# Kernel tuning notes

Hardware: AMD Instinct MI355X
Metric: run time of the kernel (lower is better)

## Reference

```python
import jax, jax.numpy as jnp
import numpy as np

N = 50000        # nodes
E = 800000       # edges
IN_DIM, HID, OUT = 512, 256, 128
EPS = 1e-5       # PyG LayerNorm eps (added to std)


def setup_inputs() -> dict:
    key = jax.random.key(0)
    ks = jax.random.split(key, 24)
    def lin(k, i, o, scale=0.05):
        kw, kb = jax.random.split(k)
        return (jax.random.normal(kw, (i, o), jnp.float32) * scale,
                jax.random.normal(kb, (o,), jnp.float32) * scale)
    x = jax.random.normal(ks[0], (N, IN_DIM), jnp.float32)
    edge_index = jax.random.randint(ks[1], (2, E), 0, N, jnp.int64)
    Wq1, bq1 = lin(ks[2], IN_DIM, HID)
    Wk1, bk1 = lin(ks[3], IN_DIM, HID)
    Wv1, bv1 = lin(ks[4], IN_DIM, HID)
    Ws1, bs1 = lin(ks[5], IN_DIM, HID)
    g1 = jnp.ones((HID,), jnp.float32)
    be1 = jnp.zeros((HID,), jnp.float32)
    Wq2, bq2 = lin(ks[6], HID, OUT)
    Wk2, bk2 = lin(ks[7], HID, OUT)
    Wv2, bv2 = lin(ks[8], HID, OUT)
    Ws2, bs2 = lin(ks[9], HID, OUT)
    g2 = jnp.ones((OUT,), jnp.float32)
    be2 = jnp.zeros((OUT,), jnp.float32)
    return dict(x=x, Wq1=Wq1, bq1=bq1, Wk1=Wk1, bk1=bk1, Wv1=Wv1, bv1=bv1,
                Ws1=Ws1, bs1=bs1, g1=g1, be1=be1,
                Wq2=Wq2, bq2=bq2, Wk2=Wk2, bk2=bk2, Wv2=Wv2, bv2=bv2,
                Ws2=Ws2, bs2=bs2, g2=g2, be2=be2, edge_index=edge_index)


def transformer_conv(x, edge_index, Wq, bq, Wk, bk, Wv, bv, Ws, bs):
    # PyG TransformerConv, heads=1, concat=True, root_weight=True
    src, dst = edge_index[0], edge_index[1]
    n = x.shape[0]
    d = Wq.shape[1]
    q = x @ Wq + bq                               # [N, d]
    k = x @ Wk + bk
    v = x @ Wv + bv
    score = (q[dst] * k[src]).sum(-1) / jnp.sqrt(jnp.asarray(d, x.dtype))  # [E]
    m = jax.ops.segment_max(score, dst, num_segments=n)     # per-target max
    e = jnp.exp(score - m[dst])
    denom = jax.ops.segment_sum(e, dst, num_segments=n)
    alpha = e / denom[dst]                         # scatter-softmax over in-edges
    agg = jax.ops.segment_sum(alpha[:, None] * v[src], dst, num_segments=n)
    return agg + (x @ Ws + bs)                     # root/skip connection


def graph_layer_norm(h, w, b):
    # PyG LayerNorm mode='graph', no batch: normalize over ALL entries
    h = h - h.mean()
    return h / (h.std() + EPS) * w + b


def reference(x, Wq1, bq1, Wk1, bk1, Wv1, bv1, Ws1, bs1, g1, be1,
              Wq2, bq2, Wk2, bk2, Wv2, bv2, Ws2, bs2, g2, be2, edge_index):
    a1 = graph_layer_norm(
        transformer_conv(x, edge_index, Wq1, bq1, Wk1, bk1, Wv1, bv1, Ws1, bs1),
        g1, be1)
    h1 = jax.nn.elu(a1)  # ELU(alpha=1.0)
    h2 = graph_layer_norm(
        transformer_conv(h1, edge_index, Wq2, bq2, Wk2, bk2, Wv2, bv2, Ws2, bs2),
        g2, be2)
    return h2
```

## Files before the change

### kernel.cpp

```cpp
#include <hip/hip_runtime.h>
#include <stdint.h>
#include <math.h>

#define IN_DIM 512
#define HID    256
#define OUTD   128
#define LN_EPS 1e-5f

typedef unsigned short u16;
typedef unsigned int   u32;
typedef short short8 __attribute__((ext_vector_type(8)));
typedef float f32x4  __attribute__((ext_vector_type(4)));

__device__ __forceinline__ float bf2f(u32 h) {
  union { u32 u; float f; } c; c.u = h << 16; return c.f;
}
__device__ __forceinline__ u16 f2bf(float f) {
  union { float f; u32 u; } c; c.f = f;
  u32 u = c.u;
  return (u16)((u + 0x7FFFu + ((u >> 16) & 1u)) >> 16);
}

__device__ __forceinline__ void gload_lds16(const void* g, void* l) {
  __builtin_amdgcn_global_load_lds((const __attribute__((address_space(1))) void*)g,
                                   (__attribute__((address_space(3))) void*)l, 16, 0, 0);
}

__global__ void k_prep(const float* __restrict__ x, u16* __restrict__ x_bf, int n4,
                       const float* __restrict__ bq1, const float* __restrict__ bk1,
                       const float* __restrict__ bv1, const float* __restrict__ bs1,
                       const float* __restrict__ bq2, const float* __restrict__ bk2,
                       const float* __restrict__ bv2, const float* __restrict__ bs2,
                       float* __restrict__ bc1, float* __restrict__ bc2) {
  int id = blockIdx.x * blockDim.x + threadIdx.x;
  if (id < n4) {
    const float4 v = ((const float4*)x)[id];
    ushort4 o;
    o.x = f2bf(v.x); o.y = f2bf(v.y); o.z = f2bf(v.z); o.w = f2bf(v.w);
    ((ushort4*)x_bf)[id] = o;
    return;
  }
  id -= n4;
  if (id < 4 * HID) {
    const float* s = (id < HID) ? bq1 : (id < 2 * HID) ? bk1 : (id < 3 * HID) ? bv1 : bs1;
    bc1[id] = s[id & (HID - 1)];
    return;
  }
  id -= 4 * HID;
  if (id < 4 * OUTD) {
    const float* s = (id < OUTD) ? bq2 : (id < 2 * OUTD) ? bk2 : (id < 3 * OUTD) ? bv2 : bs2;
    bc2[id] = s[id & (OUTD - 1)];
  }
}

__global__ void k_transpose4(const float* __restrict__ s0, const float* __restrict__ s1,
                             const float* __restrict__ s2, const float* __restrict__ s3,
                             u16* __restrict__ out, int K, int Nw) {
  __shared__ u16 t[32][33];
  const float* src = (blockIdx.z == 0) ? s0 : (blockIdx.z == 1) ? s1
                     : (blockIdx.z == 2) ? s2 : s3;
  u16* dst = out + (size_t)blockIdx.z * K * Nw;
  int k0 = blockIdx.x * 32, n0 = blockIdx.y * 32;
  int tx = threadIdx.x, ty = threadIdx.y;
#pragma unroll
  for (int i = 0; i < 32; i += 8)
    t[ty + i][tx] = f2bf(src[(size_t)(k0 + ty + i) * Nw + n0 + tx]);
  __syncthreads();
#pragma unroll
  for (int i = 0; i < 32; i += 8)
    dst[(size_t)(n0 + ty + i) * K + k0 + tx] = t[tx][ty + i];
}

__global__ void k_hist(const int* __restrict__ dst, int* __restrict__ deg, int E) {
  int e = blockIdx.x * blockDim.x + threadIdx.x;
  if (e < E) atomicAdd(&deg[dst[e]], 1);
}

__global__ void k_block_sum(const int* __restrict__ deg, int* __restrict__ bsum, int n) {
  __shared__ int sm[256];
  int i = blockIdx.x * 256 + threadIdx.x;
  sm[threadIdx.x] = (i < n) ? deg[i] : 0;
  __syncthreads();
  for (int off = 128; off > 0; off >>= 1) {
    if (threadIdx.x < off) sm[threadIdx.x] += sm[threadIdx.x + off];
    __syncthreads();
  }
  if (threadIdx.x == 0) bsum[blockIdx.x] = sm[0];
}

__global__ void k_scan_bsum(const int* __restrict__ bsum, int* __restrict__ boff, int nb) {
  __shared__ int sm[256];
  int t = threadIdx.x;
  int v = (t < nb) ? bsum[t] : 0;
  sm[t] = v;
  __syncthreads();
  for (int off = 1; off < 256; off <<= 1) {
    int tmp = (t >= off) ? sm[t - off] : 0;
    __syncthreads();
    sm[t] += tmp;
    __syncthreads();
  }
  if (t < nb) boff[t] = sm[t] - v;
}

__global__ void k_scan_final(const int* __restrict__ deg, const int* __restrict__ boff,
                             int* __restrict__ offsets, int* __restrict__ cur,
                             int n, int total) {
  __shared__ int sm[256];
  int t = threadIdx.x;
  int i = blockIdx.x * 256 + t;
  int v = (i < n) ? deg[i] : 0;
  sm[t] = v;
  __syncthreads();
  for (int off = 1; off < 256; off <<= 1) {
    int tmp = (t >= off) ? sm[t - off] : 0;
    __syncthreads();
    sm[t] += tmp;
    __syncthreads();
  }
  if (i < n) {
    int o = boff[blockIdx.x] + sm[t] - v;
    offsets[i] = o;
    cur[i] = o;
  }
  if (i == 0) offsets[n] = total;
}

__global__ void k_scatter(const int* __restrict__ src, const int* __restrict__ dst,
                          int* __restrict__ cursor, int* __restrict__ ssrc, int E) {
  int e = blockIdx.x * blockDim.x + threadIdx.x;
  if (e >= E) return;
  int d = dst[e];
  int pos = atomicAdd(&cursor[d], 1);
  ssrc[pos] = src[e];
}

__global__ __launch_bounds__(256) void k_gemm_bf16_nt(
    const u16* __restrict__ A, const u16* __restrict__ Bt, const float* __restrict__ bias,
    u16* __restrict__ C, int M, int K, int Nt) {
  __shared__ __align__(16) u16 As[128 * 32];
  __shared__ __align__(16) u16 Bs[128 * 32];
  const int tid = threadIdx.x;
  const int bm0 = blockIdx.x * 128;
  const int bn0 = blockIdx.y * 128;
  const int wave = tid >> 6, lane = tid & 63;
  const int q = lane >> 4, r16 = lane & 15;
  const int wm = (wave >> 1) * 64, wn = (wave & 1) * 64;

  f32x4 acc[4][4];
#pragma unroll
  for (int i = 0; i < 4; i++)
#pragma unroll
    for (int j = 0; j < 4; j++) acc[i][j] = (f32x4){0.f, 0.f, 0.f, 0.f};

  const int r0 = tid >> 2;
  const int c0 = (tid & 3) * 8;

  for (int kt = 0; kt < K; kt += 32) {
#pragma unroll
    for (int h = 0; h < 2; ++h) {
      int row = r0 + h * 64;
      gload_lds16(A + (size_t)(bm0 + row) * K + kt + c0, &As[row * 32 + c0]);
      gload_lds16(Bt + (size_t)(bn0 + row) * K + kt + c0, &Bs[row * 32 + c0]);
    }
    __syncthreads();
    short8 af[4], bfr[4];
#pragma unroll
    for (int i = 0; i < 4; i++) af[i] = *(const short8*)(&As[(wm + i * 16 + r16) * 32 + q * 8]);
#pragma unroll
    for (int j = 0; j < 4; j++) bfr[j] = *(const short8*)(&Bs[(wn + j * 16 + r16) * 32 + q * 8]);
#pragma unroll
    for (int i = 0; i < 4; i++)
#pragma unroll
      for (int j = 0; j < 4; j++)
        acc[i][j] = __builtin_amdgcn_mfma_f32_16x16x32_bf16(af[i], bfr[j], acc[i][j], 0, 0, 0);
    __syncthreads();
  }

#pragma unroll
  for (int i = 0; i < 4; i++) {
#pragma unroll
    for (int r = 0; r < 4; r++) {
      int grow = bm0 + wm + i * 16 + q * 4 + r;
      if (grow >= M) continue;
      size_t rbase = (size_t)grow * Nt;
#pragma unroll
      for (int j = 0; j < 4; j++) {
        int gcol = bn0 + wn + j * 16 + r16;
        float v = acc[i][j][r] + bias[gcol];
        C[rbase + gcol] = f2bf(v);
      }
    }
  }
}

template <int VPL>
__device__ __forceinline__ void load_bf(const u16* __restrict__ p, int lane, float* f) {
  if constexpr (VPL == 4) {
    uint2 r = *(const uint2*)(p + lane * 4);
    f[0] = bf2f(r.x & 0xffffu); f[1] = bf2f(r.x >> 16);
    f[2] = bf2f(r.y & 0xffffu); f[3] = bf2f(r.y >> 16);
  } else {
    u32 r = *(const u32*)(p + lane * 2);
    f[0] = bf2f(r & 0xffffu); f[1] = bf2f(r >> 16);
  }
}

template <int H, bool OUT_BF16>
__global__ __launch_bounds__(256) void k_conv(
    const u16* __restrict__ qkvs, const int* __restrict__ offsets,
    const int* __restrict__ ssrc, u16* __restrict__ out_bf,
    float* __restrict__ out_f, int n, float scale) {
  constexpr int VPL = H / 64;
  int gw = (blockIdx.x * blockDim.x + threadIdx.x) >> 6;
  int lane = threadIdx.x & 63;
  if (gw >= n) return;
  const u16* base = qkvs + (size_t)gw * (4 * H);
  float qf[VPL];
  load_bf<VPL>(base, lane, qf);
  int beg = offsets[gw], end = offsets[gw + 1];
  float m = -INFINITY, l = 0.f;
  float agg[VPL];
#pragma unroll
  for (int w = 0; w < VPL; w++) agg[w] = 0.f;

  int i = beg;
  for (; i + 4 <= end; i += 4) {
    int s0 = ssrc[i], s1 = ssrc[i + 1], s2 = ssrc[i + 2], s3 = ssrc[i + 3];
    const u16* k0p = qkvs + (size_t)s0 * (4 * H) + H;
    const u16* k1p = qkvs + (size_t)s1 * (4 * H) + H;
    const u16* k2p = qkvs + (size_t)s2 * (4 * H) + H;
    const u16* k3p = qkvs + (size_t)s3 * (4 * H) + H;
    float k0[VPL], k1[VPL], k2[VPL], k3[VPL];
    float v0[VPL], v1[VPL], v2[VPL], v3[VPL];
    load_bf<VPL>(k0p, lane, k0);
    load_bf<VPL>(k1p, lane, k1);
    load_bf<VPL>(k2p, lane, k2);
    load_bf<VPL>(k3p, lane, k3);
    load_bf<VPL>(k0p + H, lane, v0);
    load_bf<VPL>(k1p + H, lane, v1);
    load_bf<VPL>(k2p + H, lane, v2);
    load_bf<VPL>(k3p + H, lane, v3);
    float d0 = 0.f, d1 = 0.f, d2 = 0.f, d3 = 0.f;
#pragma unroll
    for (int w = 0; w < VPL; w++) {
      d0 += qf[w] * k0[w]; d1 += qf[w] * k1[w];
      d2 += qf[w] * k2[w]; d3 += qf[w] * k3[w];
    }
#pragma unroll
    for (int off = 32; off > 0; off >>= 1) {
      d0 += __shfl_xor(d0, off, 64);
      d1 += __shfl_xor(d1, off, 64);
      d2 += __shfl_xor(d2, off, 64);
      d3 += __shfl_xor(d3, off, 64);
    }
    d0 *= scale; d1 *= scale; d2 *= scale; d3 *= scale;
    float cm = fmaxf(fmaxf(d0, d1), fmaxf(d2, d3));
    float nm = fmaxf(m, cm);
    float sc = __expf(m - nm);
    float p0 = __expf(d0 - nm), p1 = __expf(d1 - nm);
    float p2 = __expf(d2 - nm), p3 = __expf(d3 - nm);
    m = nm;
    l = l * sc + (p0 + p1) + (p2 + p3);
#pragma unroll
    for (int w = 0; w < VPL; w++)
      agg[w] = agg[w] * sc + p0 * v0[w] + p1 * v1[w] + p2 * v2[w] + p3 * v3[w];
  }
  for (; i < end; ++i) {
    int s = ssrc[i];
    const u16* kb = qkvs + (size_t)s * (4 * H) + H;
    float kf[VPL], vf[VPL];
    load_bf<VPL>(kb, lane, kf);
    load_bf<VPL>(kb + H, lane, vf);
    float d = 0.f;
#pragma unroll
    for (int w = 0; w < VPL; w++) d += qf[w] * kf[w];
#pragma unroll
    for (int off = 32; off > 0; off >>= 1) d += __shfl_xor(d, off, 64);
    float score = d * scale;
    float nm = fmaxf(m, score);
    float sc = __expf(m - nm);
    float p = __expf(score - nm);
    m = nm;
    l = l * sc + p;
#pragma unroll
    for (int w = 0; w < VPL; w++) agg[w] = agg[w] * sc + p * vf[w];
  }

  float sf[VPL];
  load_bf<VPL>(base + 3 * H, lane, sf);
  float inv = (end > beg) ? 1.f / l : 0.f;
#pragma unroll
  for (int w = 0; w < VPL; w++) {
    float r = agg[w] * inv + sf[w];
    if (OUT_BF16) out_bf[(size_t)gw * H + lane * VPL + w] = f2bf(r);
    else out_f[(size_t)gw * H + lane * VPL + w] = r;
  }
}

__global__ void k_stats_bf16(const u16* __restrict__ a, int n8, double* __restrict__ st) {
  float s = 0.f, s2 = 0.f;
  for (int i = blockIdx.x * blockDim.x + threadIdx.x; i < n8; i += gridDim.x * blockDim.x) {
    uint4 v = ((const uint4*)a)[i];
    const u32 va[4] = {v.x, v.y, v.z, v.w};
#pragma unroll
    for (int w = 0; w < 4; w++) {
      float x0 = bf2f(va[w] & 0xffffu), x1 = bf2f(va[w] >> 16);
      s += x0 + x1; s2 += x0 * x0 + x1 * x1;
    }
  }
  __shared__ float sm[256], sm2[256];
  sm[threadIdx.x] = s; sm2[threadIdx.x] = s2;
  __syncthreads();
  for (int off = 128; off > 0; off >>= 1) {
    if (threadIdx.x < off) { sm[threadIdx.x] += sm[threadIdx.x + off]; sm2[threadIdx.x] += sm2[threadIdx.x + off]; }
    __syncthreads();
  }
  if (threadIdx.x == 0) { atomicAdd(&st[0], (double)sm[0]); atomicAdd(&st[1], (double)sm2[0]); }
}

__global__ void k_stats_f32(const float* __restrict__ a, int n4, double* __restrict__ st) {
  float s = 0.f, s2 = 0.f;
  for (int i = blockIdx.x * blockDim.x + threadIdx.x; i < n4; i += gridDim.x * blockDim.x) {
    float4 v = ((const float4*)a)[i];
    s += v.x + v.y + v.z + v.w;
    s2 += v.x * v.x + v.y * v.y + v.z * v.z + v.w * v.w;
  }
  __shared__ float sm[256], sm2[256];
  sm[threadIdx.x] = s; sm2[threadIdx.x] = s2;
  __syncthreads();
  for (int off = 128; off > 0; off >>= 1) {
    if (threadIdx.x < off) { sm[threadIdx.x] += sm[threadIdx.x + off]; sm2[threadIdx.x] += sm2[threadIdx.x + off]; }
    __syncthreads();
  }
  if (threadIdx.x == 0) { atomicAdd(&st[0], (double)sm[0]); atomicAdd(&st[1], (double)sm2[0]); }
}

__global__ void k_finstats(const double* __restrict__ st, float* __restrict__ fs, double cnt) {
  double mu = st[0] / cnt;
  double var = st[1] / cnt - mu * mu;
  if (var < 0.0) var = 0.0;
  fs[0] = (float)mu;
  fs[1] = (float)(1.0 / (sqrt(var) + (double)LN_EPS));
}

__global__ void k_norm_elu_bf16(const u16* __restrict__ a, const float* __restrict__ g,
                                const float* __restrict__ b, const float* __restrict__ fs,
                                u16* __restrict__ out, int n8, int Hmask) {
  int id = blockIdx.x * blockDim.x + threadIdx.x;
  if (id >= n8) return;
  int i8 = id * 8;
  int cb = i8 & Hmask;
  uint4 v = *(const uint4*)(a + i8);
  const u32 va[4] = {v.x, v.y, v.z, v.w};
  float mu = fs[0], inv = fs[1];
  uint4 o;
  u32* op = (u32*)&o;
#pragma unroll
  for (int w = 0; w < 4; w++) {
    float y0 = (bf2f(va[w] & 0xffffu) - mu) * inv * g[cb + 2 * w] + b[cb + 2 * w];
    float y1 = (bf2f(va[w] >> 16) - mu) * inv * g[cb + 2 * w + 1] + b[cb + 2 * w + 1];
    y0 = (y0 > 0.f) ? y0 : (__expf(y0) - 1.f);
    y1 = (y1 > 0.f) ? y1 : (__expf(y1) - 1.f);
    op[w] = (u32)f2bf(y0) | ((u32)f2bf(y1) << 16);
  }
  *(uint4*)(out + i8) = o;
}

__global__ void k_norm_f32(float* __restrict__ a, const float* __restrict__ g,
                           const float* __restrict__ b, const float* __restrict__ fs,
                           int n4, int Hmask) {
  int id = blockIdx.x * blockDim.x + threadIdx.x;
  if (id >= n4) return;
  int i4 = id * 4;
  int cb = i4 & Hmask;
  float4 v = *(const float4*)(a + i4);
  float mu = fs[0], inv = fs[1];
  float4 o;
  o.x = (v.x - mu) * inv * g[cb] + b[cb];
  o.y = (v.y - mu) * inv * g[cb + 1] + b[cb + 1];
  o.z = (v.z - mu) * inv * g[cb + 2] + b[cb + 2];
  o.w = (v.w - mu) * inv * g[cb + 3] + b[cb + 3];
  *(float4*)(a + i4) = o;
}

extern "C" void kernel_launch(void* const* d_in, const int* in_sizes, int n_in,
                              void* d_out, int out_size, void* d_ws, size_t ws_size,
                              hipStream_t stream) {
  const float* x   = (const float*)d_in[0];
  const float* Wq1 = (const float*)d_in[1];  const float* bq1 = (const float*)d_in[2];
  const float* Wk1 = (const float*)d_in[3];  const float* bk1 = (const float*)d_in[4];
  const float* Wv1 = (const float*)d_in[5];  const float* bv1 = (const float*)d_in[6];
  const float* Ws1 = (const float*)d_in[7];  const float* bs1 = (const float*)d_in[8];
  const float* g1  = (const float*)d_in[9];  const float* be1 = (const float*)d_in[10];
  const float* Wq2 = (const float*)d_in[11]; const float* bq2 = (const float*)d_in[12];
  const float* Wk2 = (const float*)d_in[13]; const float* bk2 = (const float*)d_in[14];
  const float* Wv2 = (const float*)d_in[15]; const float* bv2 = (const float*)d_in[16];
  const float* Ws2 = (const float*)d_in[17]; const float* bs2 = (const float*)d_in[18];
  const float* g2  = (const float*)d_in[19]; const float* be2 = (const float*)d_in[20];
  const int*   ei  = (const int*)d_in[21];

  const int N = in_sizes[0] / IN_DIM;
  const int E = in_sizes[21] / 2;
  const int* esrc = ei;
  const int* edst = ei + E;

  char* w = (char*)d_ws;
  auto carve = [&](size_t bytes) { char* p = w; w += (bytes + 255) & ~(size_t)255; return p; };
  int* deg   = (int*)carve((size_t)(N + 1) * 4);
  double* st = (double*)carve(64);
  u16* x_bf  = (u16*)carve((size_t)N * IN_DIM * 2);
  u16* Wt1   = (u16*)carve((size_t)4 * HID * IN_DIM * 2);
  u16* Wt2   = (u16*)carve((size_t)4 * OUTD * HID * 2);
  float* bc1 = (float*)carve(4 * HID * 4);
  float* bc2 = (float*)carve(4 * OUTD * 4);
  u16* qkvs1 = (u16*)carve((size_t)N * 4 * HID * 2);
  u16* a1    = (u16*)carve((size_t)N * HID * 2);
  int* offs  = (int*)carve((size_t)(N + 1) * 4);
  int* cur   = (int*)carve((size_t)(N + 1) * 4);
  int* ssrc  = (int*)carve((size_t)E * 4);
  int* bsum  = (int*)carve(1024);
  int* boff  = (int*)carve(1024);
  float* fs  = (float*)carve(64);
  u16* h1    = x_bf;
  u16* qkvs2 = qkvs1;

  hipMemsetAsync(deg, 0, (size_t)((char*)st - (char*)deg) + 64, stream);

  int n4 = N * IN_DIM / 4;
  int prep_total = n4 + 4 * HID + 4 * OUTD;
  k_prep<<<(prep_total + 255) / 256, 256, 0, stream>>>(
      x, x_bf, n4, bq1, bk1, bv1, bs1, bq2, bk2, bv2, bs2, bc1, bc2);
  dim3 tb(32, 8);
  dim3 tg1(IN_DIM / 32, HID / 32, 4);
  k_transpose4<<<tg1, tb, 0, stream>>>(Wq1, Wk1, Wv1, Ws1, Wt1, IN_DIM, HID);
  dim3 tg2(HID / 32, OUTD / 32, 4);
  k_transpose4<<<tg2, tb, 0, stream>>>(Wq2, Wk2, Wv2, Ws2, Wt2, HID, OUTD);

  int nb = (N + 255) / 256;
  k_hist<<<(E + 255) / 256, 256, 0, stream>>>(edst, deg, E);
  k_block_sum<<<nb, 256, 0, stream>>>(deg, bsum, N);
  k_scan_bsum<<<1, 256, 0, stream>>>(bsum, boff, nb);
  k_scan_final<<<nb, 256, 0, stream>>>(deg, boff, offs, cur, N, E);
  k_scatter<<<(E + 255) / 256, 256, 0, stream>>>(esrc, edst, cur, ssrc, E);

  dim3 gg1((N + 127) / 128, (4 * HID) / 128);
  k_gemm_bf16_nt<<<gg1, 256, 0, stream>>>(x_bf, Wt1, bc1, qkvs1, N, IN_DIM, 4 * HID);
  k_conv<HID, true><<<(N + 3) / 4, 256, 0, stream>>>(qkvs1, offs, ssrc, a1, nullptr, N,
                                                     1.0f / sqrtf((float)HID));
  k_stats_bf16<<<2048, 256, 0, stream>>>(a1, N * HID / 8, st);
  k_finstats<<<1, 1, 0, stream>>>(st, fs, (double)N * HID);
  k_norm_elu_bf16<<<(N * HID / 8 + 255) / 256, 256, 0, stream>>>(a1, g1, be1, fs, h1,
                                                                 N * HID / 8, HID - 1);

  dim3 gg2((N + 127) / 128, (4 * OUTD) / 128);
  k_gemm_bf16_nt<<<gg2, 256, 0, stream>>>(h1, Wt2, bc2, qkvs2, N, HID, 4 * OUTD);
  k_conv<OUTD, false><<<(N + 3) / 4, 256, 0, stream>>>(qkvs2, offs, ssrc, nullptr, (float*)d_out,
                                                       N, 1.0f / sqrtf((float)OUTD));
  k_stats_f32<<<2048, 256, 0, stream>>>((const float*)d_out, N * OUTD / 4, st + 2);
  k_finstats<<<1, 1, 0, stream>>>(st + 2, fs + 2, (double)N * OUTD);
  k_norm_f32<<<(N * OUTD / 4 + 255) / 256, 256, 0, stream>>>((float*)d_out, g2, be2, fs + 2,
                                                             N * OUTD / 4, OUTD - 1);
}
```

Before: 734.1 us.

## Fuse prep kernels, single-block scan, merge scatter into GEMM, fold stats into conv

Merges the x conversion, degree histogram, bias copy and both weight transposes into one multi-role launch. Replaces the three-kernel prefix scan with a single 1024-thread block scan. Appends the CSR scatter blocks to the first GEMM grid and remaps GEMM tiles with an XCD-aware swizzle. Computes the LayerNorm sum and sum of squares inside the conv kernel from its register results, and has the norm kernels derive mean and std from the raw sums, which removes the separate stats and finstats kernels. The cost is a serial single-block scan and extra per-block double atomics in conv. There is also an ordering risk: the scatter writes ssrc while sharing a launch with the GEMM, which is safe only because the GEMM does not read ssrc.

```diff
diff --git a/kernel.cpp b/kernel.cpp
--- a/kernel.cpp
+++ b/kernel.cpp
@@ -26,123 +26,136 @@
                                    (__attribute__((address_space(3))) void*)l, 16, 0, 0);
 }
 
-__global__ void k_prep(const float* __restrict__ x, u16* __restrict__ x_bf, int n4,
-                       const float* __restrict__ bq1, const float* __restrict__ bk1,
-                       const float* __restrict__ bv1, const float* __restrict__ bs1,
-                       const float* __restrict__ bq2, const float* __restrict__ bk2,
-                       const float* __restrict__ bv2, const float* __restrict__ bs2,
-                       float* __restrict__ bc1, float* __restrict__ bc2) {
-  int id = blockIdx.x * blockDim.x + threadIdx.x;
-  if (id < n4) {
-    const float4 v = ((const float4*)x)[id];
-    ushort4 o;
-    o.x = f2bf(v.x); o.y = f2bf(v.y); o.z = f2bf(v.z); o.w = f2bf(v.w);
-    ((ushort4*)x_bf)[id] = o;
+__global__ __launch_bounds__(256) void k_prep(
+    const float* __restrict__ x, u16* __restrict__ x_bf, int n4,
+    const int* __restrict__ edst, int* __restrict__ deg, int E,
+    const float* __restrict__ bq1, const float* __restrict__ bk1,
+    const float* __restrict__ bv1, const float* __restrict__ bs1,
+    const float* __restrict__ bq2, const float* __restrict__ bk2,
+    const float* __restrict__ bv2, const float* __restrict__ bs2,
+    float* __restrict__ bc1, float* __restrict__ bc2,
+    const float* __restrict__ Wq1, const float* __restrict__ Wk1,
+    const float* __restrict__ Wv1, const float* __restrict__ Ws1,
+    const float* __restrict__ Wq2, const float* __restrict__ Wk2,
+    const float* __restrict__ Wv2, const float* __restrict__ Ws2,
+    u16* __restrict__ Wt1, u16* __restrict__ Wt2,
+    int b_cvt, int b_hist) {
+  __shared__ u16 t[32][33];
+  int blk = blockIdx.x;
+  int tid = threadIdx.x;
+  if (blk < b_cvt) {
+    int id = blk * 256 + tid;
+    if (id < n4) {
+      const float4 v = ((const float4*)x)[id];
+      ushort4 o;
+      o.x = f2bf(v.x); o.y = f2bf(v.y); o.z = f2bf(v.z); o.w = f2bf(v.w);
+      ((ushort4*)x_bf)[id] = o;
+    }
     return;
   }
-  id -= n4;
-  if (id < 4 * HID) {
-    const float* s = (id < HID) ? bq1 : (id < 2 * HID) ? bk1 : (id < 3 * HID) ? bv1 : bs1;
-    bc1[id] = s[id & (HID - 1)];
+  blk -= b_cvt;
+  if (blk < b_hist) {
+    int e = blk * 256 + tid;
+    if (e < E) atomicAdd(&deg[edst[e]], 1);
     return;
   }
-  id -= 4 * HID;
-  if (id < 4 * OUTD) {
-    const float* s = (id < OUTD) ? bq2 : (id < 2 * OUTD) ? bk2 : (id < 3 * OUTD) ? bv2 : bs2;
-    bc2[id] = s[id & (OUTD - 1)];
-  }
-}
-
-__global__ void k_transpose4(const float* __restrict__ s0, const float* __restrict__ s1,
-                             const float* __restrict__ s2, const float* __restrict__ s3,
-                             u16* __restrict__ out, int K, int Nw) {
-  __shared__ u16 t[32][33];
-  const float* src = (blockIdx.z == 0) ? s0 : (blockIdx.z == 1) ? s1
-                     : (blockIdx.z == 2) ? s2 : s3;
-  u16* dst = out + (size_t)blockIdx.z * K * Nw;
-  int k0 = blockIdx.x * 32, n0 = blockIdx.y * 32;
-  int tx = threadIdx.x, ty = threadIdx.y;
-#pragma unroll
-  for (int i = 0; i < 32; i += 8)
-    t[ty + i][tx] = f2bf(src[(size_t)(k0 + ty + i) * Nw + n0 + tx]);
+  blk -= b_hist;
+  if (blk < 6) {
+    int id = blk * 256 + tid;
+    if (id < 4 * HID) {
+      const float* s = (id < HID) ? bq1 : (id < 2 * HID) ? bk1 : (id < 3 * HID) ? bv1 : bs1;
+      bc1[id] = s[id & (HID - 1)];
+    } else if (id < 4 * HID + 4 * OUTD) {
+      int j = id - 4 * HID;
+      const float* s = (j < OUTD) ? bq2 : (j < 2 * OUTD) ? bk2 : (j < 3 * OUTD) ? bv2 : bs2;
+      bc2[j] = s[j & (OUTD - 1)];
+    }
+    return;
+  }
+  blk -= 6;
+  int tx = tid & 31, ty = tid >> 5;
+  if (blk < 512) {
+    int mat = blk >> 7, r = blk & 127;
+    int k0 = (r >> 3) * 32, n0 = (r & 7) * 32;
+    const float* src = (mat == 0) ? Wq1 : (mat == 1) ? Wk1 : (mat == 2) ? Wv1 : Ws1;
+    u16* dst = Wt1 + (size_t)mat * IN_DIM * HID;
+#pragma unroll
+    for (int i = 0; i < 32; i += 8)
+      t[ty + i][tx] = f2bf(src[(size_t)(k0 + ty + i) * HID + n0 + tx]);
+    __syncthreads();
+#pragma unroll
+    for (int i = 0; i < 32; i += 8)
+      dst[(size_t)(n0 + ty + i) * IN_DIM + k0 + tx] = t[tx][ty + i];
+    return;
+  }
+  blk -= 512;
+  {
+    int mat = blk >> 5, r = blk & 31;
+    int k0 = (r >> 2) * 32, n0 = (r & 3) * 32;
+    const float* src = (mat == 0) ? Wq2 : (mat == 1) ? Wk2 : (mat == 2) ? Wv2 : Ws2;
+    u16* dst = Wt2 + (size_t)mat * HID * OUTD;
+#pragma unroll
+    for (int i = 0; i < 32; i += 8)
+      t[ty + i][tx] = f2bf(src[(size_t)(k0 + ty + i) * OUTD + n0 + tx]);
+    __syncthreads();
+#pragma unroll
+    for (int i = 0; i < 32; i += 8)
+      dst[(size_t)(n0 + ty + i) * HID + k0 + tx] = t[tx][ty + i];
+  }
+}
+
+__global__ __launch_bounds__(1024) void k_scan(const int* __restrict__ deg,
+                                               int* __restrict__ offsets,
+                                               int* __restrict__ cur, int n, int total) {
+  __shared__ int sm[1024];
+  int t = threadIdx.x;
+  int chunk = (n + 1023) / 1024;
+  int base = t * chunk;
+  int s = 0;
+  for (int i = base; i < base + chunk && i < n; ++i) s += deg[i];
+  sm[t] = s;
   __syncthreads();
-#pragma unroll
-  for (int i = 0; i < 32; i += 8)
-    dst[(size_t)(n0 + ty + i) * K + k0 + tx] = t[tx][ty + i];
-}
-
-__global__ void k_hist(const int* __restrict__ dst, int* __restrict__ deg, int E) {
-  int e = blockIdx.x * blockDim.x + threadIdx.x;
-  if (e < E) atomicAdd(&deg[dst[e]], 1);
-}
-
-__global__ void k_block_sum(const int* __restrict__ deg, int* __restrict__ bsum, int n) {
-  __shared__ int sm[256];
-  int i = blockIdx.x * 256 + threadIdx.x;
-  sm[threadIdx.x] = (i < n) ? deg[i] : 0;
-  __syncthreads();
-  for (int off = 128; off > 0; off >>= 1) {
-    if (threadIdx.x < off) sm[threadIdx.x] += sm[threadIdx.x + off];
-    __syncthreads();
-  }
-  if (threadIdx.x == 0) bsum[blockIdx.x] = sm[0];
-}
-
-__global__ void k_scan_bsum(const int* __restrict__ bsum, int* __restrict__ boff, int nb) {
-  __shared__ int sm[256];
-  int t = threadIdx.x;
-  int v = (t < nb) ? bsum[t] : 0;
-  sm[t] = v;
-  __syncthreads();
-  for (int off = 1; off < 256; off <<= 1) {
-    int tmp = (t >= off) ? sm[t - off] : 0;
-    __syncthreads();
-    sm[t] += tmp;
-    __syncthreads();
-  }
-  if (t < nb) boff[t] = sm[t] - v;
-}
-
-__global__ void k_scan_final(const int* __restrict__ deg, const int* __restrict__ boff,
-                             int* __restrict__ offsets, int* __restrict__ cur,
-                             int n, int total) {
-  __shared__ int sm[256];
-  int t = threadIdx.x;
-  int i = blockIdx.x * 256 + t;
-  int v = (i < n) ? deg[i] : 0;
-  sm[t] = v;
-  __syncthreads();
-  for (int off = 1; off < 256; off <<= 1) {
-    int tmp = (t >= off) ? sm[t - off] : 0;
-    __syncthreads();
-    sm[t] += tmp;
-    __syncthreads();
-  }
-  if (i < n) {
-    int o = boff[blockIdx.x] + sm[t] - v;
-    offsets[i] = o;
-    cur[i] = o;
-  }
-  if (i == 0) offsets[n] = total;
-}
-
-__global__ void k_scatter(const int* __restrict__ src, const int* __restrict__ dst,
-                          int* __restrict__ cursor, int* __restrict__ ssrc, int E) {
-  int e = blockIdx.x * blockDim.x + threadIdx.x;
-  if (e >= E) return;
-  int d = dst[e];
-  int pos = atomicAdd(&cursor[d], 1);
-  ssrc[pos] = src[e];
-}
-
-__global__ __launch_bounds__(256) void k_gemm_bf16_nt(
+  for (int off = 1; off < 1024; off <<= 1) {
+    int v = (t >= off) ? sm[t - off] : 0;
+    __syncthreads();
+    sm[t] += v;
+    __syncthreads();
+  }
+  int run = sm[t] - s;
+  for (int i = base; i < base + chunk && i < n; ++i) {
+    offsets[i] = run;
+    cur[i] = run;
+    run += deg[i];
+  }
+  if (t == 0) offsets[n] = total;
+}
+
+__global__ __launch_bounds__(256) void k_gemm_sc(
     const u16* __restrict__ A, const u16* __restrict__ Bt, const float* __restrict__ bias,
-    u16* __restrict__ C, int M, int K, int Nt) {
+    u16* __restrict__ C, int M, int K, int Nt, int nbn, int gemm_blocks,
+    const int* __restrict__ esrc, const int* __restrict__ edst,
+    int* __restrict__ cur, int* __restrict__ ssrc, int E) {
+  if ((int)blockIdx.x >= gemm_blocks) {
+    int e = (blockIdx.x - gemm_blocks) * 256 + threadIdx.x;
+    if (e < E) {
+      int d = edst[e];
+      int pos = atomicAdd(&cur[d], 1);
+      ssrc[pos] = esrc[e];
+    }
+    return;
+  }
+  int bid = blockIdx.x;
+  int xcd = bid & 7;
+  int nm = bid >> 3;
+  int n = nm % nbn;
+  int m = (nm / nbn) * 8 + xcd;
+  if (m * 128 >= M) return;
+
   __shared__ __align__(16) u16 As[128 * 32];
   __shared__ __align__(16) u16 Bs[128 * 32];
   const int tid = threadIdx.x;
-  const int bm0 = blockIdx.x * 128;
-  const int bn0 = blockIdx.y * 128;
+  const int bm0 = m * 128;
+  const int bn0 = n * 128;
   const int wave = tid >> 6, lane = tid & 63;
   const int q = lane >> 4, r16 = lane & 15;
   const int wm = (wave >> 1) * 64, wn = (wave & 1) * 64;
@@ -210,150 +223,134 @@
 __global__ __launch_bounds__(256) void k_conv(
     const u16* __restrict__ qkvs, const int* __restrict__ offsets,
     const int* __restrict__ ssrc, u16* __restrict__ out_bf,
-    float* __restrict__ out_f, int n, float scale) {
+    float* __restrict__ out_f, int n, float scale, double* __restrict__ st) {
   constexpr int VPL = H / 64;
   int gw = (blockIdx.x * blockDim.x + threadIdx.x) >> 6;
+  int wave = threadIdx.x >> 6;
   int lane = threadIdx.x & 63;
-  if (gw >= n) return;
-  const u16* base = qkvs + (size_t)gw * (4 * H);
-  float qf[VPL];
-  load_bf<VPL>(base, lane, qf);
-  int beg = offsets[gw], end = offsets[gw + 1];
-  float m = -INFINITY, l = 0.f;
-  float agg[VPL];
-#pragma unroll
-  for (int w = 0; w < VPL; w++) agg[w] = 0.f;
-
-  int i = beg;
-  for (; i + 4 <= end; i += 4) {
-    int s0 = ssrc[i], s1 = ssrc[i + 1], s2 = ssrc[i + 2], s3 = ssrc[i + 3];
-    const u16* k0p = qkvs + (size_t)s0 * (4 * H) + H;
-    const u16* k1p = qkvs + (size_t)s1 * (4 * H) + H;
-    const u16* k2p = qkvs + (size_t)s2 * (4 * H) + H;
-    const u16* k3p = qkvs + (size_t)s3 * (4 * H) + H;
-    float k0[VPL], k1[VPL], k2[VPL], k3[VPL];
-    float v0[VPL], v1[VPL], v2[VPL], v3[VPL];
-    load_bf<VPL>(k0p, lane, k0);
-    load_bf<VPL>(k1p, lane, k1);
-    load_bf<VPL>(k2p, lane, k2);
-    load_bf<VPL>(k3p, lane, k3);
-    load_bf<VPL>(k0p + H, lane, v0);
-    load_bf<VPL>(k1p + H, lane, v1);
-    load_bf<VPL>(k2p + H, lane, v2);
-    load_bf<VPL>(k3p + H, lane, v3);
-    float d0 = 0.f, d1 = 0.f, d2 = 0.f, d3 = 0.f;
-#pragma unroll
-    for (int w = 0; w < VPL; w++) {
-      d0 += qf[w] * k0[w]; d1 += qf[w] * k1[w];
-      d2 += qf[w] * k2[w]; d3 += qf[w] * k3[w];
-    }
-#pragma unroll
-    for (int off = 32; off > 0; off >>= 1) {
-      d0 += __shfl_xor(d0, off, 64);
-      d1 += __shfl_xor(d1, off, 64);
-      d2 += __shfl_xor(d2, off, 64);
-      d3 += __shfl_xor(d3, off, 64);
-    }
-    d0 *= scale; d1 *= scale; d2 *= scale; d3 *= scale;
-    float cm = fmaxf(fmaxf(d0, d1), fmaxf(d2, d3));
-    float nm = fmaxf(m, cm);
-    float sc = __expf(m - nm);
-    float p0 = __expf(d0 - nm), p1 = __expf(d1 - nm);
-    float p2 = __expf(d2 - nm), p3 = __expf(d3 - nm);
-    m = nm;
-    l = l * sc + (p0 + p1) + (p2 + p3);
-#pragma unroll
-    for (int w = 0; w < VPL; w++)
-      agg[w] = agg[w] * sc + p0 * v0[w] + p1 * v1[w] + p2 * v2[w] + p3 * v3[w];
-  }
-  for (; i < end; ++i) {
-    int s = ssrc[i];
-    const u16* kb = qkvs + (size_t)s * (4 * H) + H;
-    float kf[VPL], vf[VPL];
-    load_bf<VPL>(kb, lane, kf);
-    load_bf<VPL>(kb + H, lane, vf);
-    float d = 0.f;
-#pragma unroll
-    for (int w = 0; w < VPL; w++) d += qf[w] * kf[w];
-#pragma unroll
-    for (int off = 32; off > 0; off >>= 1) d += __shfl_xor(d, off, 64);
-    float score = d * scale;
-    float nm = fmaxf(m, score);
-    float sc = __expf(m - nm);
-    float p = __expf(score - nm);
-    m = nm;
-    l = l * sc + p;
-#pragma unroll
-    for (int w = 0; w < VPL; w++) agg[w] = agg[w] * sc + p * vf[w];
-  }
-
-  float sf[VPL];
-  load_bf<VPL>(base + 3 * H, lane, sf);
-  float inv = (end > beg) ? 1.f / l : 0.f;
-#pragma unroll
-  for (int w = 0; w < VPL; w++) {
-    float r = agg[w] * inv + sf[w];
-    if (OUT_BF16) out_bf[(size_t)gw * H + lane * VPL + w] = f2bf(r);
-    else out_f[(size_t)gw * H + lane * VPL + w] = r;
-  }
-}
-
-__global__ void k_stats_bf16(const u16* __restrict__ a, int n8, double* __restrict__ st) {
+  bool live = gw < n;
+  float r[VPL];
+#pragma unroll
+  for (int w = 0; w < VPL; w++) r[w] = 0.f;
+
+  if (live) {
+    const u16* base = qkvs + (size_t)gw * (4 * H);
+    float qf[VPL];
+    load_bf<VPL>(base, lane, qf);
+    int beg = offsets[gw], end = offsets[gw + 1];
+    float m = -INFINITY, l = 0.f;
+    float agg[VPL];
+#pragma unroll
+    for (int w = 0; w < VPL; w++) agg[w] = 0.f;
+
+    int i = beg;
+    for (; i + 4 <= end; i += 4) {
+      int s0 = ssrc[i], s1 = ssrc[i + 1], s2 = ssrc[i + 2], s3 = ssrc[i + 3];
+      const u16* k0p = qkvs + (size_t)s0 * (4 * H) + H;
+      const u16* k1p = qkvs + (size_t)s1 * (4 * H) + H;
+      const u16* k2p = qkvs + (size_t)s2 * (4 * H) + H;
+      const u16* k3p = qkvs + (size_t)s3 * (4 * H) + H;
+      float k0[VPL], k1[VPL], k2[VPL], k3[VPL];
+      float v0[VPL], v1[VPL], v2[VPL], v3[VPL];
+      load_bf<VPL>(k0p, lane, k0);
+      load_bf<VPL>(k1p, lane, k1);
+      load_bf<VPL>(k2p, lane, k2);
+      load_bf<VPL>(k3p, lane, k3);
+      load_bf<VPL>(k0p + H, lane, v0);
+      load_bf<VPL>(k1p + H, lane, v1);
+      load_bf<VPL>(k2p + H, lane, v2);
+      load_bf<VPL>(k3p + H, lane, v3);
+      float d0 = 0.f, d1 = 0.f, d2 = 0.f, d3 = 0.f;
+#pragma unroll
+      for (int w = 0; w < VPL; w++) {
+        d0 += qf[w] * k0[w]; d1 += qf[w] * k1[w];
+        d2 += qf[w] * k2[w]; d3 += qf[w] * k3[w];
+      }
+#pragma unroll
+      for (int off = 32; off > 0; off >>= 1) {
+        d0 += __shfl_xor(d0, off, 64);
+        d1 += __shfl_xor(d1, off, 64);
+        d2 += __shfl_xor(d2, off, 64);
+        d3 += __shfl_xor(d3, off, 64);
+      }
+      d0 *= scale; d1 *= scale; d2 *= scale; d3 *= scale;
+      float cm = fmaxf(fmaxf(d0, d1), fmaxf(d2, d3));
+      float nm = fmaxf(m, cm);
+      float sc = __expf(m - nm);
+      float p0 = __expf(d0 - nm), p1 = __expf(d1 - nm);
+      float p2 = __expf(d2 - nm), p3 = __expf(d3 - nm);
+      m = nm;
+      l = l * sc + (p0 + p1) + (p2 + p3);
+#pragma unroll
+      for (int w = 0; w < VPL; w++)
+        agg[w] = agg[w] * sc + p0 * v0[w] + p1 * v1[w] + p2 * v2[w] + p3 * v3[w];
+    }
+    for (; i < end; ++i) {
+      int s = ssrc[i];
+      const u16* kb = qkvs + (size_t)s * (4 * H) + H;
+      float kf[VPL], vf[VPL];
+      load_bf<VPL>(kb, lane, kf);
+      load_bf<VPL>(kb + H, lane, vf);
+      float d = 0.f;
+#pragma unroll
+      for (int w = 0; w < VPL; w++) d += qf[w] * kf[w];
+#pragma unroll
+      for (int off = 32; off > 0; off >>= 1) d += __shfl_xor(d, off, 64);
+      float score = d * scale;
+      float nm = fmaxf(m, score);
+      float sc = __expf(m - nm);
+      float p = __expf(score - nm);
+      m = nm;
+      l = l * sc + p;
+#pragma unroll
+      for (int w = 0; w < VPL; w++) agg[w] = agg[w] * sc + p * vf[w];
+    }
+
+    float sf[VPL];
+    load_bf<VPL>(base + 3 * H, lane, sf);
+    float inv = (end > beg) ? 1.f / l : 0.f;
+#pragma unroll
+    for (int w = 0; w < VPL; w++) r[w] = agg[w] * inv + sf[w];
+    if (OUT_BF16) {
+#pragma unroll
+      for (int w = 0; w < VPL; w++) out_bf[(size_t)gw * H + lane * VPL + w] = f2bf(r[w]);
+    } else {
+#pragma unroll
+      for (int w = 0; w < VPL; w++) out_f[(size_t)gw * H + lane * VPL + w] = r[w];
+    }
+  }
+
   float s = 0.f, s2 = 0.f;
-  for (int i = blockIdx.x * blockDim.x + threadIdx.x; i < n8; i += gridDim.x * blockDim.x) {
-    uint4 v = ((const uint4*)a)[i];
-    const u32 va[4] = {v.x, v.y, v.z, v.w};
-#pragma unroll
-    for (int w = 0; w < 4; w++) {
-      float x0 = bf2f(va[w] & 0xffffu), x1 = bf2f(va[w] >> 16);
-      s += x0 + x1; s2 += x0 * x0 + x1 * x1;
-    }
-  }
-  __shared__ float sm[256], sm2[256];
-  sm[threadIdx.x] = s; sm2[threadIdx.x] = s2;
+#pragma unroll
+  for (int w = 0; w < VPL; w++) { s += r[w]; s2 += r[w] * r[w]; }
+#pragma unroll
+  for (int off = 32; off > 0; off >>= 1) {
+    s += __shfl_xor(s, off, 64);
+    s2 += __shfl_xor(s2, off, 64);
+  }
+  __shared__ float bsm[8];
+  if (lane == 0) { bsm[wave * 2] = s; bsm[wave * 2 + 1] = s2; }
   __syncthreads();
-  for (int off = 128; off > 0; off >>= 1) {
-    if (threadIdx.x < off) { sm[threadIdx.x] += sm[threadIdx.x + off]; sm2[threadIdx.x] += sm2[threadIdx.x + off]; }
-    __syncthreads();
-  }
-  if (threadIdx.x == 0) { atomicAdd(&st[0], (double)sm[0]); atomicAdd(&st[1], (double)sm2[0]); }
-}
-
-__global__ void k_stats_f32(const float* __restrict__ a, int n4, double* __restrict__ st) {
-  float s = 0.f, s2 = 0.f;
-  for (int i = blockIdx.x * blockDim.x + threadIdx.x; i < n4; i += gridDim.x * blockDim.x) {
-    float4 v = ((const float4*)a)[i];
-    s += v.x + v.y + v.z + v.w;
-    s2 += v.x * v.x + v.y * v.y + v.z * v.z + v.w * v.w;
-  }
-  __shared__ float sm[256], sm2[256];
-  sm[threadIdx.x] = s; sm2[threadIdx.x] = s2;
-  __syncthreads();
-  for (int off = 128; off > 0; off >>= 1) {
-    if (threadIdx.x < off) { sm[threadIdx.x] += sm[threadIdx.x + off]; sm2[threadIdx.x] += sm2[threadIdx.x + off]; }
-    __syncthreads();
-  }
-  if (threadIdx.x == 0) { atomicAdd(&st[0], (double)sm[0]); atomicAdd(&st[1], (double)sm2[0]); }
-}
-
-__global__ void k_finstats(const double* __restrict__ st, float* __restrict__ fs, double cnt) {
-  double mu = st[0] / cnt;
-  double var = st[1] / cnt - mu * mu;
-  if (var < 0.0) var = 0.0;
-  fs[0] = (float)mu;
-  fs[1] = (float)(1.0 / (sqrt(var) + (double)LN_EPS));
+  if (threadIdx.x == 0) {
+    atomicAdd(&st[0], (double)(bsm[0] + bsm[2] + bsm[4] + bsm[6]));
+    atomicAdd(&st[1], (double)(bsm[1] + bsm[3] + bsm[5] + bsm[7]));
+  }
 }
 
 __global__ void k_norm_elu_bf16(const u16* __restrict__ a, const float* __restrict__ g,
-                                const float* __restrict__ b, const float* __restrict__ fs,
-                                u16* __restrict__ out, int n8, int Hmask) {
+                                const float* __restrict__ b, const double* __restrict__ st,
+                                double cnt, u16* __restrict__ out, int n8, int Hmask) {
   int id = blockIdx.x * blockDim.x + threadIdx.x;
   if (id >= n8) return;
+  double mud = st[0] / cnt;
+  double var = st[1] / cnt - mud * mud;
+  if (var < 0.0) var = 0.0;
+  float mu = (float)mud;
+  float inv = (float)(1.0 / (sqrt(var) + (double)LN_EPS));
   int i8 = id * 8;
   int cb = i8 & Hmask;
   uint4 v = *(const uint4*)(a + i8);
   const u32 va[4] = {v.x, v.y, v.z, v.w};
-  float mu = fs[0], inv = fs[1];
   uint4 o;
   u32* op = (u32*)&o;
 #pragma unroll
@@ -368,14 +365,18 @@
 }
 
 __global__ void k_norm_f32(float* __restrict__ a, const float* __restrict__ g,
-                           const float* __restrict__ b, const float* __restrict__ fs,
-                           int n4, int Hmask) {
+                           const float* __restrict__ b, const double* __restrict__ st,
+                           double cnt, int n4, int Hmask) {
   int id = blockIdx.x * blockDim.x + threadIdx.x;
   if (id >= n4) return;
+  double mud = st[0] / cnt;
+  double var = st[1] / cnt - mud * mud;
+  if (var < 0.0) var = 0.0;
+  float mu = (float)mud;
+  float inv = (float)(1.0 / (sqrt(var) + (double)LN_EPS));
   int i4 = id * 4;
   int cb = i4 & Hmask;
   float4 v = *(const float4*)(a + i4);
-  float mu = fs[0], inv = fs[1];
   float4 o;
   o.x = (v.x - mu) * inv * g[cb] + b[cb];
   o.y = (v.y - mu) * inv * g[cb + 1] + b[cb + 1];
@@ -419,46 +420,41 @@
   int* offs  = (int*)carve((size_t)(N + 1) * 4);
   int* cur   = (int*)carve((size_t)(N + 1) * 4);
   int* ssrc  = (int*)carve((size_t)E * 4);
-  int* bsum  = (int*)carve(1024);
-  int* boff  = (int*)carve(1024);
-  float* fs  = (float*)carve(64);
   u16* h1    = x_bf;
   u16* qkvs2 = qkvs1;
 
   hipMemsetAsync(deg, 0, (size_t)((char*)st - (char*)deg) + 64, stream);
 
   int n4 = N * IN_DIM / 4;
-  int prep_total = n4 + 4 * HID + 4 * OUTD;
-  k_prep<<<(prep_total + 255) / 256, 256, 0, stream>>>(
-      x, x_bf, n4, bq1, bk1, bv1, bs1, bq2, bk2, bv2, bs2, bc1, bc2);
-  dim3 tb(32, 8);
-  dim3 tg1(IN_DIM / 32, HID / 32, 4);
-  k_transpose4<<<tg1, tb, 0, stream>>>(Wq1, Wk1, Wv1, Ws1, Wt1, IN_DIM, HID);
-  dim3 tg2(HID / 32, OUTD / 32, 4);
-  k_transpose4<<<tg2, tb, 0, stream>>>(Wq2, Wk2, Wv2, Ws2, Wt2, HID, OUTD);
-
-  int nb = (N + 255) / 256;
-  k_hist<<<(E + 255) / 256, 256, 0, stream>>>(edst, deg, E);
-  k_block_sum<<<nb, 256, 0, stream>>>(deg, bsum, N);
-  k_scan_bsum<<<1, 256, 0, stream>>>(bsum, boff, nb);
-  k_scan_final<<<nb, 256, 0, stream>>>(deg, boff, offs, cur, N, E);
-  k_scatter<<<(E + 255) / 256, 256, 0, stream>>>(esrc, edst, cur, ssrc, E);
-
-  dim3 gg1((N + 127) / 128, (4 * HID) / 128);
-  k_gemm_bf16_nt<<<gg1, 256, 0, stream>>>(x_bf, Wt1, bc1, qkvs1, N, IN_DIM, 4 * HID);
+  int b_cvt = (n4 + 255) / 256;
+  int b_hist = (E + 255) / 256;
+  int k1_blocks = b_cvt + b_hist + 6 + 512 + 128;
+  k_prep<<<k1_blocks, 256, 0, stream>>>(
+      x, x_bf, n4, edst, deg, E,
+      bq1, bk1, bv1, bs1, bq2, bk2, bv2, bs2, bc1, bc2,
+      Wq1, Wk1, Wv1, Ws1, Wq2, Wk2, Wv2, Ws2, Wt1, Wt2, b_cvt, b_hist);
+
+  k_scan<<<1, 1024, 0, stream>>>(deg, offs, cur, N, E);
+
+  int mblk = (N + 127) / 128;
+  int grp = (mblk + 7) / 8;
+  int g1_blocks = grp * 8 * 8;
+  k_gemm_sc<<<g1_blocks + b_hist, 256, 0, stream>>>(
+      x_bf, Wt1, bc1, qkvs1, N, IN_DIM, 4 * HID, 8, g1_blocks,
+      esrc, edst, cur, ssrc, E);
+
   k_conv<HID, true><<<(N + 3) / 4, 256, 0, stream>>>(qkvs1, offs, ssrc, a1, nullptr, N,
-                                                     1.0f / sqrtf((float)HID));
-  k_stats_bf16<<<2048, 256, 0, stream>>>(a1, N * HID / 8, st);
-  k_finstats<<<1, 1, 0, stream>>>(st, fs, (double)N * HID);
-  k_norm_elu_bf16<<<(N * HID / 8 + 255) / 256, 256, 0, stream>>>(a1, g1, be1, fs, h1,
-                                                                 N * HID / 8, HID - 1);
-
-  dim3 gg2((N + 127) / 128, (4 * OUTD) / 128);
-  k_gemm_bf16_nt<<<gg2, 256, 0, stream>>>(h1, Wt2, bc2, qkvs2, N, HID, 4 * OUTD);
+                                                     1.0f / sqrtf((float)HID), st);
+  k_norm_elu_bf16<<<(N * HID / 8 + 255) / 256, 256, 0, stream>>>(
+      a1, g1, be1, st, (double)N * HID, h1, N * HID / 8, HID - 1);
+
+  int g2_blocks = grp * 8 * 4;
+  k_gemm_sc<<<g2_blocks, 256, 0, stream>>>(
+      h1, Wt2, bc2, qkvs2, N, HID, 4 * OUTD, 4, g2_blocks,
+      nullptr, nullptr, nullptr, nullptr, 0);
+
   k_conv<OUTD, false><<<(N + 3) / 4, 256, 0, stream>>>(qkvs2, offs, ssrc, nullptr, (float*)d_out,
-                                                       N, 1.0f / sqrtf((float)OUTD));
-  k_stats_f32<<<2048, 256, 0, stream>>>((const float*)d_out, N * OUTD / 4, st + 2);
-  k_finstats<<<1, 1, 0, stream>>>(st + 2, fs + 2, (double)N * OUTD);
-  k_norm_f32<<<(N * OUTD / 4 + 255) / 256, 256, 0, stream>>>((float*)d_out, g2, be2, fs + 2,
-                                                             N * OUTD / 4, OUTD - 1);
-}
+                                                       N, 1.0f / sqrtf((float)OUTD), st + 2);
+  k_norm_f32<<<(N * OUTD / 4 + 255) / 256, 256, 0, stream>>>(
+      (float*)d_out, g2, be2, st + 2, (double)N * OUTD, N * OUTD / 4, OUTD - 1);
+}
```

Result: slower. 1.154 ms (+57.2%).
